# Kernel optimization log

Hardware: AMD Instinct MI355X
Metric: run time of the kernel (lower is better)

## Reference

```python
import jax, jax.numpy as jnp
import numpy as np

B, C, H, W = 256, 3, 128, 128
K = 16                      # vae_small.img_size == kernel == stride (non-overlapping)
GH, GW = H // K, W // K
P = C * K * K               # 768 flattened patch dim
HID = 2048
L = 256                     # latent_size


def setup_inputs() -> dict:
    key = jax.random.key(0)
    ks = jax.random.split(key, 9)
    s = 0.02
    f32 = jnp.float32
    return {
        "x": jax.random.uniform(ks[0], (B, C, H, W), f32),
        "w_enc1": jax.random.normal(ks[1], (P, HID), f32) * s,
        "b_enc1": jnp.zeros((HID,), f32),
        "w_enc2": jax.random.normal(ks[2], (HID, 2 * L), f32) * s,
        "b_enc2": jnp.zeros((2 * L,), f32),
        "w_dec1": jax.random.normal(ks[3], (L, HID), f32) * s,
        "b_dec1": jnp.zeros((HID,), f32),
        "w_dec2": jax.random.normal(ks[4], (HID, P), f32) * s,
        "b_dec2": jnp.zeros((P,), f32),
    }


def reference(x, w_enc1, b_enc1, w_enc2, b_enc2, w_dec1, b_dec1, w_dec2, b_dec2):
    b, c, h, w = x.shape
    gh, gw = h // K, w // K
    # unfold: [b,c,h,w] -> [b,gh,gw, c*K*K]  (same padding is 0 when stride==k)
    patches = (x.reshape(b, c, gh, K, gw, K)
                .transpose(0, 2, 4, 1, 3, 5)
                .reshape(b, gh, gw, c * K * K))
    # batched per-patch VAE encode (replaces the python map/unbind loop)
    he = jax.nn.relu(patches @ w_enc1 + b_enc1)            # [b,gh,gw,HID]
    mu_logvar = he @ w_enc2 + b_enc2                        # [b,gh,gw,2L]
    mu = mu_logvar[..., :L]
    z = mu                                                  # deterministic reparameterize
    # batched per-patch decode
    hd = jax.nn.relu(z @ w_dec1 + b_dec1)                   # [b,gh,gw,HID]
    dec = jax.nn.sigmoid(hd @ w_dec2 + b_dec2)              # [b,gh,gw,P]
    # fold: exact inverse of unfold since stride == kernel
    recon_x = (dec.reshape(b, gh, gw, c, K, K)
                 .transpose(0, 3, 1, 4, 2, 5)
                 .reshape(b, c, h, w))
    mu_logvar_2d = jnp.transpose(mu_logvar, (0, 3, 1, 2))   # [b, 2L, gh, gw]
    return recon_x, mu_logvar_2d
```

## Files before the change

### kernel.cpp

```cpp
#include <hip/hip_runtime.h>
#include <hip/hip_bf16.h>
#include <stdint.h>

typedef __bf16 bf16x8_t __attribute__((ext_vector_type(8)));
typedef float f32x4_t __attribute__((ext_vector_type(4)));
typedef unsigned short ushort8_t __attribute__((ext_vector_type(8)));

__device__ __forceinline__ unsigned short f2bf(float f) {
    union { float f; uint32_t i; } v; v.f = f;
    uint32_t i = v.i + (((v.i >> 16) & 1u) + 0x7FFFu);
    return (unsigned short)(i >> 16);
}

typedef const __attribute__((address_space(1))) void* gas_t;
typedef __attribute__((address_space(3))) void* las_t;
__device__ __forceinline__ void load_lds16(const unsigned short* g, unsigned short* l) {
    __builtin_amdgcn_global_load_lds((gas_t)g, (las_t)l, 16, 0, 0);
}

#define BB   256
#define CC   3
#define HH   128
#define WW   128
#define PP   768
#define HID  2048
#define LL   256
#define MM   16384

__global__ void patchify(const float* __restrict__ x,
                         unsigned short* __restrict__ patches) {
    int t = blockIdx.x * 256 + threadIdx.x;
    int e = t * 8;
    int col = e & 127;
    int row = (e >> 7) & 127;
    int c   = (e >> 14) % 3;
    int b   = e / (128 * 128 * 3);
    int gh = row >> 4, kh = row & 15, gw = col >> 4, kw = col & 15;
    long po = (long)(b * 64 + gh * 8 + gw) * PP + c * 256 + kh * 16 + kw;
    float4 v0 = *(const float4*)(x + e);
    float4 v1 = *(const float4*)(x + e + 4);
    ushort8_t o;
    o[0] = f2bf(v0.x); o[1] = f2bf(v0.y); o[2] = f2bf(v0.z); o[3] = f2bf(v0.w);
    o[4] = f2bf(v1.x); o[5] = f2bf(v1.y); o[6] = f2bf(v1.z); o[7] = f2bf(v1.w);
    *(ushort8_t*)(patches + po) = o;
}

__global__ void transpose_k(const float* __restrict__ in,
                            unsigned short* __restrict__ out, int R, int C) {
    __shared__ unsigned short tile[32][34];
    int nbc = C >> 5;
    int tc = blockIdx.x % nbc, tr = blockIdx.x / nbc;
    int tx = threadIdx.x & 31, ty0 = threadIdx.x >> 5;
    int r0 = tr << 5, c0 = tc << 5;
    #pragma unroll
    for (int i = 0; i < 4; ++i) {
        int ty = ty0 + i * 8;
        tile[ty][tx] = f2bf(in[(long)(r0 + ty) * C + c0 + tx]);
    }
    __syncthreads();
    #pragma unroll
    for (int i = 0; i < 4; ++i) {
        int ty = ty0 + i * 8;
        out[(long)(c0 + ty) * R + r0 + tx] = tile[tx][ty];
    }
}

#define BMT 256
#define BNT 128
#define BKT 32
#define LDS_TILE ((BMT + BNT) * BKT)

template <int ACT, int WMODE>
__global__ void __launch_bounds__(512)
gemm_bt(const unsigned short* __restrict__ A, int lda,
        const unsigned short* __restrict__ Bt,
        const float* __restrict__ bias,
        unsigned short* __restrict__ C0u,
        float* __restrict__ C0f,
        float* __restrict__ C1f,
        int ldc, int Kd, int nbn, int m0) {
    __shared__ __align__(16) unsigned short lds_buf[4 * LDS_TILE];
    const int nbm = gridDim.x / nbn;
    const int stripe = nbm >> 3;
    const int xcd = blockIdx.x & 7;
    const int loc = blockIdx.x >> 3;
    const int bm = xcd * stripe + (loc % stripe);
    const int bn = loc / stripe;
    const int tid = threadIdx.x;
    const int wave = tid >> 6;
    const int lane = tid & 63;
    const int wr = wave >> 1;
    const int wc = wave & 1;
    const int fr = lane & 15;
    const int quad = lane >> 4;

    const int Gl = tid ^ ((tid >> 3) & 7);
    const int sr = Gl >> 2;
    const int sg = (Gl & 3) << 3;

    const unsigned short* Ab = A + (long)bm * BMT * lda;
    const unsigned short* Bb = Bt + (long)bn * BNT * Kd;

    int gA[4], gB[4];
    #pragma unroll
    for (int i = 0; i < 4; ++i) {
        const int r = (wr << 6) + (i << 4) + fr;
        gA[i] = ((((r << 2) | quad) ^ ((r >> 1) & 7)) << 3);
    }
    #pragma unroll
    for (int j = 0; j < 4; ++j) {
        const int r = (wc << 6) + (j << 4) + fr;
        gB[j] = ((((r << 2) | quad) ^ ((r >> 1) & 7)) << 3);
    }

    f32x4_t acc[4][4];
    #pragma unroll
    for (int i = 0; i < 4; ++i)
        #pragma unroll
        for (int j = 0; j < 4; ++j)
            acc[i][j] = (f32x4_t){0.f, 0.f, 0.f, 0.f};

    const int nt = Kd / BKT;

    #define STAGE(t) do {                                                      \
        unsigned short* Al_ = lds_buf + ((t) & 3) * LDS_TILE;                  \
        unsigned short* Bl_ = Al_ + BMT * BKT;                                 \
        const long k0_ = (long)(t) * BKT;                                      \
        load_lds16(Ab + (long)sr * lda + k0_ + sg,         Al_ + (wave << 9)); \
        load_lds16(Ab + (long)(sr + 128) * lda + k0_ + sg,                     \
                   Al_ + 4096 + (wave << 9));                                  \
        load_lds16(Bb + (long)sr * Kd + k0_ + sg,          Bl_ + (wave << 9)); \
    } while (0)

    STAGE(0);
    STAGE(1);
    asm volatile("s_waitcnt vmcnt(3)" ::: "memory");
    __builtin_amdgcn_s_barrier();
    __builtin_amdgcn_sched_barrier(0);

    for (int t = 0; t < nt; ++t) {
        if (t + 2 < nt) STAGE(t + 2);
        const unsigned short* Al = lds_buf + (t & 3) * LDS_TILE;
        const unsigned short* Bl = Al + BMT * BKT;
        bf16x8_t af[4], bfr[4];
        #pragma unroll
        for (int i = 0; i < 4; ++i) af[i] = *(const bf16x8_t*)&Al[gA[i]];
        #pragma unroll
        for (int j = 0; j < 4; ++j) bfr[j] = *(const bf16x8_t*)&Bl[gB[j]];
        __builtin_amdgcn_s_setprio(1);
        #pragma unroll
        for (int i = 0; i < 4; ++i)
            #pragma unroll
            for (int j = 0; j < 4; ++j)
                acc[i][j] = __builtin_amdgcn_mfma_f32_16x16x32_bf16(
                    af[i], bfr[j], acc[i][j], 0, 0, 0);
        __builtin_amdgcn_s_setprio(0);
        if (t + 1 < nt) {
            if (t + 2 < nt) asm volatile("s_waitcnt vmcnt(3)" ::: "memory");
            else            asm volatile("s_waitcnt vmcnt(0)" ::: "memory");
            __builtin_amdgcn_s_barrier();
            __builtin_amdgcn_sched_barrier(0);
        }
    }
    #undef STAGE

    const int gcol0 = bn * BNT + (wc << 6);
    const int grow0 = bm * BMT + (wr << 6);
    #pragma unroll
    for (int j = 0; j < 4; ++j) {
        const int n = gcol0 + (j << 4) + fr;
        const float bv = bias[n];
        #pragma unroll
        for (int i = 0; i < 4; ++i) {
            #pragma unroll
            for (int r = 0; r < 4; ++r) {
                const int m = grow0 + (i << 4) + (quad << 2) + r;
                float v = acc[i][j][r] + bv;
                if (ACT == 1) v = fmaxf(v, 0.f);
                if (ACT == 2) v = 1.f / (1.f + __expf(-v));
                if (WMODE == 0) {
                    C0u[(long)m * ldc + n] = f2bf(v);
                } else if (WMODE == 1) {
                    const int gm = m0 + m;
                    C1f[((long)(gm >> 6) * 512 + n) * 64 + (gm & 63)] = v;
                    if (n < 256) C0u[(long)m * 256 + n] = f2bf(v);
                } else {
                    const int gm = m0 + m;
                    const int b = gm >> 6, g6 = gm & 63;
                    const int gh = g6 >> 3, gw = g6 & 7;
                    const int c = n >> 8, kh = (n >> 4) & 15, kw = n & 15;
                    const long o = (long)(b * 3 + c) * 16384
                                 + ((gh << 4) + kh) * 128 + (gw << 4) + kw;
                    C0f[o] = v;
                }
            }
        }
    }
}

extern "C" void kernel_launch(void* const* d_in, const int* in_sizes, int n_in,
                              void* d_out, int out_size, void* d_ws, size_t ws_size,
                              hipStream_t stream) {
    const float* x      = (const float*)d_in[0];
    const float* w_enc1 = (const float*)d_in[1];
    const float* b_enc1 = (const float*)d_in[2];
    const float* w_enc2 = (const float*)d_in[3];
    const float* b_enc2 = (const float*)d_in[4];
    const float* w_dec1 = (const float*)d_in[5];
    const float* b_dec1 = (const float*)d_in[6];
    const float* w_dec2 = (const float*)d_in[7];
    const float* b_dec2 = (const float*)d_in[8];
    float* outf = (float*)d_out;
    unsigned short* patches = (unsigned short*)d_out;
    float* out_ml = outf + (long)MM * PP;

    const size_t WT_ELEMS = 2048 * 768 + 512 * 2048 + 2048 * 256 + 768 * 2048;
    unsigned short* sb;
    long Mc;
    if (ws_size >= (WT_ELEMS + (size_t)MM * (LL + HID)) * 2) {
        sb = (unsigned short*)d_ws;  Mc = MM;
    } else {
        sb = (unsigned short*)d_in[0]; Mc = 8192;
    }
    unsigned short* wT1 = sb;
    unsigned short* wT2 = wT1 + 2048 * 768;
    unsigned short* wT3 = wT2 + 512 * 2048;
    unsigned short* wT4 = wT3 + 2048 * 256;
    unsigned short* mu  = wT4 + 768 * 2048;
    unsigned short* he  = mu + Mc * LL;

    patchify<<<6144, 256, 0, stream>>>(x, patches);

    transpose_k<<<(768 / 32) * (2048 / 32), 256, 0, stream>>>(w_enc1, wT1, 768, 2048);
    transpose_k<<<(2048 / 32) * (512 / 32), 256, 0, stream>>>(w_enc2, wT2, 2048, 512);
    transpose_k<<<(256 / 32) * (2048 / 32), 256, 0, stream>>>(w_dec1, wT3, 256, 2048);
    transpose_k<<<(2048 / 32) * (768 / 32), 256, 0, stream>>>(w_dec2, wT4, 2048, 768);

    const int nbm = (int)(Mc / BMT);
    for (long m0 = MM - Mc; m0 >= 0; m0 -= Mc) {
        gemm_bt<1, 0><<<nbm * (HID / BNT), 512, 0, stream>>>(
            patches + m0 * PP, PP, wT1, b_enc1,
            he, nullptr, nullptr, HID, PP, HID / BNT, 0);
        gemm_bt<0, 1><<<nbm * (512 / BNT), 512, 0, stream>>>(
            he, HID, wT2, b_enc2,
            mu, nullptr, out_ml, 0, HID, 512 / BNT, (int)m0);
        gemm_bt<1, 0><<<nbm * (HID / BNT), 512, 0, stream>>>(
            mu, LL, wT3, b_dec1,
            he, nullptr, nullptr, HID, LL, HID / BNT, 0);
        gemm_bt<2, 2><<<nbm * (PP / BNT), 512, 0, stream>>>(
            he, HID, wT4, b_dec2,
            nullptr, outf, nullptr, 0, HID, PP / BNT, (int)m0);
    }
}
```

Measured before the change: 378.2 us.

## Restructure GEMM main loop into 8-phase ping-pong schedule with BK=64

The GEMM K-loop now handles 64 elements per iteration as two 32-wide halves. Each half is split into two MFMA phases over column pairs, separated by barriers, and the global-to-LDS loads for future half-tiles are interleaved between phases. LDS is laid out as separate A and B ring buffers of four half-stages, and launch bounds request two blocks per CU. The goal is to overlap LDS reads, global loads and MFMA issue across waves more finely. The cost is many more barriers per iteration, and the hand-tuned vmcnt waits could be wrong.

```diff
diff --git a/kernel.cpp b/kernel.cpp
--- a/kernel.cpp
+++ b/kernel.cpp
@@ -67,11 +67,10 @@
 
 #define BMT 256
 #define BNT 128
-#define BKT 32
-#define LDS_TILE ((BMT + BNT) * BKT)
+#define BKT 64
 
 template <int ACT, int WMODE>
-__global__ void __launch_bounds__(512)
+__global__ void __launch_bounds__(512, 2)
 gemm_bt(const unsigned short* __restrict__ A, int lda,
         const unsigned short* __restrict__ Bt,
         const float* __restrict__ bias,
@@ -79,7 +78,7 @@
         float* __restrict__ C0f,
         float* __restrict__ C1f,
         int ldc, int Kd, int nbn, int m0) {
-    __shared__ __align__(16) unsigned short lds_buf[4 * LDS_TILE];
+    __shared__ __align__(16) unsigned short lds_buf[49152];
     const int nbm = gridDim.x / nbn;
     const int stripe = nbm >> 3;
     const int xcd = blockIdx.x & 7;
@@ -122,47 +121,84 @@
 
     const int nt = Kd / BKT;
 
-    #define STAGE(t) do {                                                      \
-        unsigned short* Al_ = lds_buf + ((t) & 3) * LDS_TILE;                  \
-        unsigned short* Bl_ = Al_ + BMT * BKT;                                 \
-        const long k0_ = (long)(t) * BKT;                                      \
-        load_lds16(Ab + (long)sr * lda + k0_ + sg,         Al_ + (wave << 9)); \
-        load_lds16(Ab + (long)(sr + 128) * lda + k0_ + sg,                     \
-                   Al_ + 4096 + (wave << 9));                                  \
-        load_lds16(Bb + (long)sr * Kd + k0_ + sg,          Bl_ + (wave << 9)); \
+    #define STAGE_HALF(k) do {                                                 \
+        const int s_ = (k) & 3;                                                \
+        unsigned short* Ad_ = lds_buf + s_ * 8192;                             \
+        unsigned short* Bd_ = lds_buf + 32768 + s_ * 4096;                     \
+        const long ko_ = (long)(k) * 32;                                       \
+        load_lds16(Ab + (long)sr * lda + ko_ + sg,         Ad_ + (wave << 9)); \
+        load_lds16(Ab + (long)(sr + 128) * lda + ko_ + sg,                     \
+                   Ad_ + 4096 + (wave << 9));                                  \
+        load_lds16(Bb + (long)sr * Kd + ko_ + sg,          Bd_ + (wave << 9)); \
     } while (0)
 
-    STAGE(0);
-    STAGE(1);
+    #define BAR() do { __builtin_amdgcn_s_barrier();                           \
+                       __builtin_amdgcn_sched_barrier(0); } while (0)
+    #define MFMA_JP(J0) do {                                                   \
+        __builtin_amdgcn_s_setprio(1);                                         \
+        _Pragma("unroll")                                                      \
+        for (int i = 0; i < 4; ++i) {                                          \
+            acc[i][J0]     = __builtin_amdgcn_mfma_f32_16x16x32_bf16(          \
+                af[i], bfr[J0],     acc[i][J0],     0, 0, 0);                  \
+            acc[i][J0 + 1] = __builtin_amdgcn_mfma_f32_16x16x32_bf16(          \
+                af[i], bfr[J0 + 1], acc[i][J0 + 1], 0, 0, 0);                  \
+        }                                                                      \
+        __builtin_amdgcn_s_setprio(0);                                         \
+    } while (0)
+
+    STAGE_HALF(0);
+    STAGE_HALF(1);
     asm volatile("s_waitcnt vmcnt(3)" ::: "memory");
-    __builtin_amdgcn_s_barrier();
-    __builtin_amdgcn_sched_barrier(0);
-
+    BAR();
+
+    bf16x8_t af[4], bfr[4];
+    #pragma unroll 2
     for (int t = 0; t < nt; ++t) {
-        if (t + 2 < nt) STAGE(t + 2);
-        const unsigned short* Al = lds_buf + (t & 3) * LDS_TILE;
-        const unsigned short* Bl = Al + BMT * BKT;
-        bf16x8_t af[4], bfr[4];
-        #pragma unroll
-        for (int i = 0; i < 4; ++i) af[i] = *(const bf16x8_t*)&Al[gA[i]];
-        #pragma unroll
-        for (int j = 0; j < 4; ++j) bfr[j] = *(const bf16x8_t*)&Bl[gB[j]];
-        __builtin_amdgcn_s_setprio(1);
-        #pragma unroll
-        for (int i = 0; i < 4; ++i)
-            #pragma unroll
-            for (int j = 0; j < 4; ++j)
-                acc[i][j] = __builtin_amdgcn_mfma_f32_16x16x32_bf16(
-                    af[i], bfr[j], acc[i][j], 0, 0, 0);
-        __builtin_amdgcn_s_setprio(0);
+        const int s0 = (t & 1) << 1;
+        const unsigned short* A0 = lds_buf + s0 * 8192;
+        const unsigned short* B0 = lds_buf + 32768 + s0 * 4096;
+        const unsigned short* A1 = A0 + 8192;
+        const unsigned short* B1 = B0 + 4096;
+
+        #pragma unroll
+        for (int i = 0; i < 4; ++i) af[i] = *(const bf16x8_t*)&A0[gA[i]];
+        bfr[0] = *(const bf16x8_t*)&B0[gB[0]];
+        bfr[1] = *(const bf16x8_t*)&B0[gB[1]];
+        if (t + 1 < nt) STAGE_HALF(2 * t + 2);
+        BAR();
+        MFMA_JP(0);
+        BAR();
+
+        bfr[2] = *(const bf16x8_t*)&B0[gB[2]];
+        bfr[3] = *(const bf16x8_t*)&B0[gB[3]];
         if (t + 1 < nt) {
-            if (t + 2 < nt) asm volatile("s_waitcnt vmcnt(3)" ::: "memory");
-            else            asm volatile("s_waitcnt vmcnt(0)" ::: "memory");
-            __builtin_amdgcn_s_barrier();
-            __builtin_amdgcn_sched_barrier(0);
+            STAGE_HALF(2 * t + 3);
+            asm volatile("s_waitcnt vmcnt(6)" ::: "memory");
+        } else {
+            asm volatile("s_waitcnt vmcnt(0)" ::: "memory");
         }
-    }
-    #undef STAGE
+        BAR();
+        MFMA_JP(2);
+        BAR();
+
+        #pragma unroll
+        for (int i = 0; i < 4; ++i) af[i] = *(const bf16x8_t*)&A1[gA[i]];
+        bfr[0] = *(const bf16x8_t*)&B1[gB[0]];
+        bfr[1] = *(const bf16x8_t*)&B1[gB[1]];
+        BAR();
+        MFMA_JP(0);
+        BAR();
+
+        bfr[2] = *(const bf16x8_t*)&B1[gB[2]];
+        bfr[3] = *(const bf16x8_t*)&B1[gB[3]];
+        asm volatile("s_waitcnt vmcnt(3)" ::: "memory");
+        BAR();
+        MFMA_JP(2);
+        BAR();
+    }
+    #undef STAGE_HALF
+    #undef BAR
+    #undef MFMA_JP
 
     const int gcol0 = bn * BNT + (wc << 6);
     const int grow0 = bm * BMT + (wr << 6);
```

Measured after the change: 395.9 us. 1.05x slower.

## Switch GEMM to 256x256x64 tiles with phased LDS reads and interleaved prefetch

Applied to the files above, without the earlier changes.

Enlarges the GEMM block tile from 256x128x32 to 256x256x64 on a 2x4 wave grid, with each wave computing a 128x64 output using 8x4 accumulators. The LDS scheme drops the four-stage ring for two buffers. Each K step is split into four MFMA phases separated by barriers, with A and B fragment reads and next-tile global-to-LDS loads spread between the phases. The aim is more data reuse per global load and memory traffic hidden behind MFMA work. The cost is more registers, 128KB of LDS per block (limiting occupancy) and many extra barriers.

```diff
diff --git a/kernel.cpp b/kernel.cpp
--- a/kernel.cpp
+++ b/kernel.cpp
@@ -66,12 +66,15 @@
 }
 
 #define BMT 256
-#define BNT 128
-#define BKT 32
-#define LDS_TILE ((BMT + BNT) * BKT)
+#define BNT 256
+#define BKT 64
+
+#define SBAR() do { __builtin_amdgcn_sched_barrier(0);                         \
+                    __builtin_amdgcn_s_barrier();                              \
+                    __builtin_amdgcn_sched_barrier(0); } while (0)
 
 template <int ACT, int WMODE>
-__global__ void __launch_bounds__(512)
+__global__ void __launch_bounds__(512, 2)
 gemm_bt(const unsigned short* __restrict__ A, int lda,
         const unsigned short* __restrict__ Bt,
         const float* __restrict__ bias,
@@ -79,7 +82,7 @@
         float* __restrict__ C0f,
         float* __restrict__ C1f,
         int ldc, int Kd, int nbn, int m0) {
-    __shared__ __align__(16) unsigned short lds_buf[4 * LDS_TILE];
+    __shared__ __align__(16) unsigned short lds_buf[65536];
     const int nbm = gridDim.x / nbn;
     const int stripe = nbm >> 3;
     const int xcd = blockIdx.x & 7;
@@ -89,89 +92,154 @@
     const int tid = threadIdx.x;
     const int wave = tid >> 6;
     const int lane = tid & 63;
-    const int wr = wave >> 1;
-    const int wc = wave & 1;
+    const int wr = wave >> 2;
+    const int wc = wave & 3;
     const int fr = lane & 15;
     const int quad = lane >> 4;
 
     const int Gl = tid ^ ((tid >> 3) & 7);
-    const int sr = Gl >> 2;
-    const int sg = (Gl & 3) << 3;
+    const int srow = Gl >> 3;
+    const int scol = (Gl & 7) << 3;
 
     const unsigned short* Ab = A + (long)bm * BMT * lda;
     const unsigned short* Bb = Bt + (long)bn * BNT * Kd;
 
-    int gA[4], gB[4];
+    const int gx0 = ((quad) ^ (fr & 7)) << 3;
+    const int gx1 = ((4 | quad) ^ (fr & 7)) << 3;
+    const int arow = fr << 6;
+    const int brow = ((wc & 1) << 12) + (fr << 6);
+
+    f32x4_t acc[8][4];
     #pragma unroll
-    for (int i = 0; i < 4; ++i) {
-        const int r = (wr << 6) + (i << 4) + fr;
-        gA[i] = ((((r << 2) | quad) ^ ((r >> 1) & 7)) << 3);
-    }
-    #pragma unroll
-    for (int j = 0; j < 4; ++j) {
-        const int r = (wc << 6) + (j << 4) + fr;
-        gB[j] = ((((r << 2) | quad) ^ ((r >> 1) & 7)) << 3);
-    }
-
-    f32x4_t acc[4][4];
-    #pragma unroll
-    for (int i = 0; i < 4; ++i)
+    for (int i = 0; i < 8; ++i)
         #pragma unroll
         for (int j = 0; j < 4; ++j)
             acc[i][j] = (f32x4_t){0.f, 0.f, 0.f, 0.f};
 
     const int nt = Kd / BKT;
 
-    #define STAGE(t) do {                                                      \
-        unsigned short* Al_ = lds_buf + ((t) & 3) * LDS_TILE;                  \
-        unsigned short* Bl_ = Al_ + BMT * BKT;                                 \
-        const long k0_ = (long)(t) * BKT;                                      \
-        load_lds16(Ab + (long)sr * lda + k0_ + sg,         Al_ + (wave << 9)); \
-        load_lds16(Ab + (long)(sr + 128) * lda + k0_ + sg,                     \
-                   Al_ + 4096 + (wave << 9));                                  \
-        load_lds16(Bb + (long)sr * Kd + k0_ + sg,          Bl_ + (wave << 9)); \
+    #define STAGE_A(kt, d) do {                                                \
+        unsigned short* a0 = lds_buf + (d) * 16384;                            \
+        const long ko_ = (long)(kt) * 64 + scol;                               \
+        load_lds16(Ab + (long)(srow)       * lda + ko_, a0 + (wave << 9));     \
+        load_lds16(Ab + (long)(srow + 64)  * lda + ko_, a0 + 4096 + (wave << 9));\
+        load_lds16(Ab + (long)(srow + 128) * lda + ko_, a0 + 8192 + (wave << 9));\
+        load_lds16(Ab + (long)(srow + 192) * lda + ko_, a0 + 12288 + (wave << 9));\
     } while (0)
-
-    STAGE(0);
-    STAGE(1);
-    asm volatile("s_waitcnt vmcnt(3)" ::: "memory");
-    __builtin_amdgcn_s_barrier();
-    __builtin_amdgcn_sched_barrier(0);
-
+    #define STAGE_B(kt, d) do {                                                \
+        unsigned short* b0 = lds_buf + 32768 + (d) * 16384;                    \
+        const long ko_ = (long)(kt) * 64 + scol;                               \
+        load_lds16(Bb + (long)(srow)       * Kd + ko_, b0 + (wave << 9));      \
+        load_lds16(Bb + (long)(srow + 64)  * Kd + ko_, b0 + 4096 + (wave << 9));\
+        load_lds16(Bb + (long)(srow + 128) * Kd + ko_, b0 + 8192 + (wave << 9));\
+        load_lds16(Bb + (long)(srow + 192) * Kd + ko_, b0 + 12288 + (wave << 9));\
+    } while (0)
+
+    STAGE_B(0, 0); STAGE_A(0, 0);
+    STAGE_B(1, 1); STAGE_A(1, 1);
+    asm volatile("s_waitcnt vmcnt(8)" ::: "memory");
+    SBAR();
+
+    bf16x8_t af[4][2], bfA[2][2], bfB[2][2];
     for (int t = 0; t < nt; ++t) {
-        if (t + 2 < nt) STAGE(t + 2);
-        const unsigned short* Al = lds_buf + (t & 3) * LDS_TILE;
-        const unsigned short* Bl = Al + BMT * BKT;
-        bf16x8_t af[4], bfr[4];
-        #pragma unroll
-        for (int i = 0; i < 4; ++i) af[i] = *(const bf16x8_t*)&Al[gA[i]];
-        #pragma unroll
-        for (int j = 0; j < 4; ++j) bfr[j] = *(const bf16x8_t*)&Bl[gB[j]];
+        const int d = t & 1;
+        const unsigned short* Ah = lds_buf + d * 16384 + wr * 8192;
+        const unsigned short* Bh = lds_buf + 32768 + d * 16384 + ((wc >> 1) << 13);
+
+        #pragma unroll
+        for (int i = 0; i < 4; ++i) {
+            af[i][0] = *(const bf16x8_t*)&Ah[arow + (i << 10) + gx0];
+            af[i][1] = *(const bf16x8_t*)&Ah[arow + (i << 10) + gx1];
+        }
+        #pragma unroll
+        for (int j = 0; j < 2; ++j) {
+            bfA[j][0] = *(const bf16x8_t*)&Bh[brow + (j << 10) + gx0];
+            bfA[j][1] = *(const bf16x8_t*)&Bh[brow + (j << 10) + gx1];
+        }
+        SBAR();
         __builtin_amdgcn_s_setprio(1);
         #pragma unroll
         for (int i = 0; i < 4; ++i)
             #pragma unroll
-            for (int j = 0; j < 4; ++j)
+            for (int j = 0; j < 2; ++j) {
                 acc[i][j] = __builtin_amdgcn_mfma_f32_16x16x32_bf16(
-                    af[i], bfr[j], acc[i][j], 0, 0, 0);
+                    af[i][0], bfA[j][0], acc[i][j], 0, 0, 0);
+                acc[i][j] = __builtin_amdgcn_mfma_f32_16x16x32_bf16(
+                    af[i][1], bfA[j][1], acc[i][j], 0, 0, 0);
+            }
         __builtin_amdgcn_s_setprio(0);
-        if (t + 1 < nt) {
-            if (t + 2 < nt) asm volatile("s_waitcnt vmcnt(3)" ::: "memory");
-            else            asm volatile("s_waitcnt vmcnt(0)" ::: "memory");
-            __builtin_amdgcn_s_barrier();
-            __builtin_amdgcn_sched_barrier(0);
-        }
-    }
-    #undef STAGE
+        SBAR();
+
+        #pragma unroll
+        for (int j = 0; j < 2; ++j) {
+            bfB[j][0] = *(const bf16x8_t*)&Bh[brow + ((j + 2) << 10) + gx0];
+            bfB[j][1] = *(const bf16x8_t*)&Bh[brow + ((j + 2) << 10) + gx1];
+        }
+        SBAR();
+        __builtin_amdgcn_s_setprio(1);
+        #pragma unroll
+        for (int i = 0; i < 4; ++i)
+            #pragma unroll
+            for (int j = 0; j < 2; ++j) {
+                acc[i][j + 2] = __builtin_amdgcn_mfma_f32_16x16x32_bf16(
+                    af[i][0], bfB[j][0], acc[i][j + 2], 0, 0, 0);
+                acc[i][j + 2] = __builtin_amdgcn_mfma_f32_16x16x32_bf16(
+                    af[i][1], bfB[j][1], acc[i][j + 2], 0, 0, 0);
+            }
+        __builtin_amdgcn_s_setprio(0);
+        SBAR();
+
+        #pragma unroll
+        for (int i = 0; i < 4; ++i) {
+            af[i][0] = *(const bf16x8_t*)&Ah[arow + ((i + 4) << 10) + gx0];
+            af[i][1] = *(const bf16x8_t*)&Ah[arow + ((i + 4) << 10) + gx1];
+        }
+        if (t + 2 < nt) STAGE_B(t + 2, d);
+        SBAR();
+        __builtin_amdgcn_s_setprio(1);
+        #pragma unroll
+        for (int i = 0; i < 4; ++i)
+            #pragma unroll
+            for (int j = 0; j < 2; ++j) {
+                acc[i + 4][j + 2] = __builtin_amdgcn_mfma_f32_16x16x32_bf16(
+                    af[i][0], bfB[j][0], acc[i + 4][j + 2], 0, 0, 0);
+                acc[i + 4][j + 2] = __builtin_amdgcn_mfma_f32_16x16x32_bf16(
+                    af[i][1], bfB[j][1], acc[i + 4][j + 2], 0, 0, 0);
+            }
+        __builtin_amdgcn_s_setprio(0);
+        SBAR();
+
+        if (t + 2 < nt) {
+            STAGE_A(t + 2, d);
+            asm volatile("s_waitcnt vmcnt(8)" ::: "memory");
+        } else if (t + 1 < nt) {
+            asm volatile("s_waitcnt vmcnt(0)" ::: "memory");
+        }
+        SBAR();
+        __builtin_amdgcn_s_setprio(1);
+        #pragma unroll
+        for (int i = 0; i < 4; ++i)
+            #pragma unroll
+            for (int j = 0; j < 2; ++j) {
+                acc[i + 4][j] = __builtin_amdgcn_mfma_f32_16x16x32_bf16(
+                    af[i][0], bfA[j][0], acc[i + 4][j], 0, 0, 0);
+                acc[i + 4][j] = __builtin_amdgcn_mfma_f32_16x16x32_bf16(
+                    af[i][1], bfA[j][1], acc[i + 4][j], 0, 0, 0);
+            }
+        __builtin_amdgcn_s_setprio(0);
+        SBAR();
+    }
+    #undef STAGE_A
+    #undef STAGE_B
 
     const int gcol0 = bn * BNT + (wc << 6);
-    const int grow0 = bm * BMT + (wr << 6);
+    const int grow0 = bm * BMT + (wr << 7);
     #pragma unroll
     for (int j = 0; j < 4; ++j) {
         const int n = gcol0 + (j << 4) + fr;
         const float bv = bias[n];
         #pragma unroll
-        for (int i = 0; i < 4; ++i) {
+        for (int i = 0; i < 8; ++i) {
             #pragma unroll
             for (int r = 0; r < 4; ++r) {
                 const int m = grow0 + (i << 4) + (quad << 2) + r;
```

Measured after the change: 429.1 us. 13.5% more time.
